# Kernel tuning notes

Hardware: AMD Instinct MI355X
Metric: run time of the kernel (lower is better)

## Reference

```python
import jax, jax.numpy as jnp
import numpy as np

DIM = 96
HEADS = 4
HID = int(DIM * 2.66)  # 255, GDFN hidden width
B, H, W = 4, 128, 128


def _conv(x, w, b=None, groups=1):
    y = jax.lax.conv_general_dilated(x, w, (1, 1), 'SAME',
                                     dimension_numbers=('NCHW', 'OIHW', 'NCHW'),
                                     feature_group_count=groups)
    return y if b is None else y + b[None, :, None, None]


def _ln(x, w, b):
    # WithBias LayerNorm over channel dim (per pixel), biased variance, eps=1e-5
    mu = x.mean(1, keepdims=True)
    var = ((x - mu) ** 2).mean(1, keepdims=True)
    return (x - mu) / jnp.sqrt(var + 1e-5) * w[None, :, None, None] + b[None, :, None, None]


def _l2norm(x):
    # torch F.normalize(dim=-1): x / max(||x||_2, 1e-12)
    return x / jnp.maximum(jnp.linalg.norm(x, axis=-1, keepdims=True), 1e-12)


def _gelu(x):
    return jax.nn.gelu(x, approximate=False)


def setup_inputs() -> dict:
    key = jax.random.key(0)
    ks = iter(jax.random.split(key, 32))
    nrm = lambda shp, s=0.02: jax.random.normal(next(ks), shp, dtype=jnp.float32) * s
    d, h2 = DIM, HID
    inp = {
        'x': jax.random.normal(next(ks), (B, DIM, H, W), dtype=jnp.float32),
        # L_conv: 3x3(d->d,+b) GELU 1x1(d->1,+b)
        'Lc_w1': nrm((d, d, 3, 3)), 'Lc_b1': jnp.zeros((d,), jnp.float32),
        'Lc_w2': nrm((1, d, 1, 1)), 'Lc_b2': jnp.zeros((1,), jnp.float32),
        # R_conv: 3x3(d->d,+b) GELU 1x1(d->3,+b)
        'Rc_w1': nrm((d, d, 3, 3)), 'Rc_b1': jnp.zeros((d,), jnp.float32),
        'Rc_w2': nrm((3, d, 1, 1)), 'Rc_b2': jnp.zeros((3,), jnp.float32),
        # L_rein: 3x3(1->d,+b) GELU ; R_rein: 3x3(3->d,+b)
        'Lr_w': nrm((d, 1, 3, 3)), 'Lr_b': jnp.zeros((d,), jnp.float32),
        'Rr_w': nrm((d, 3, 3, 3)), 'Rr_b': jnp.zeros((d,), jnp.float32),
        # LayerNorms (WithBias)
        'n1_w': jnp.ones((d,), jnp.float32), 'n1_b': jnp.zeros((d,), jnp.float32),
        'nL_w': jnp.ones((d,), jnp.float32), 'nL_b': jnp.zeros((d,), jnp.float32),
        'n2_w': jnp.ones((d,), jnp.float32), 'n2_b': jnp.zeros((d,), jnp.float32),
        # Illum_Attention (bias=False)
        'temp': jnp.ones((HEADS, 1, 1), jnp.float32),
        'q_w': nrm((d, d, 1, 1)),
        'qd_w': nrm((d, d, 3, 3)),          # q_dwconv is a FULL 3x3 conv (no groups)
        'kv_w': nrm((2 * d, d, 1, 1)),
        'kvd_w': nrm((2 * d, 1, 3, 3)),     # depthwise, groups=2*dim
        'po_w': nrm((d, d, 1, 1)),
        # FeedForward (bias=False); NOTE: 'dwconv' here is a FULL 3x3 conv
        'pi_w': nrm((h2, d, 1, 1)),
        'fdw_w': nrm((h2, h2, 3, 3)),
        'fpo_w': nrm((d, h2, 1, 1)),
    }
    return inp


def reference(x, Lc_w1, Lc_b1, Lc_w2, Lc_b2, Rc_w1, Rc_b1, Rc_w2, Rc_b2,
              Lr_w, Lr_b, Rr_w, Rr_b, n1_w, n1_b, nL_w, nL_b, n2_w, n2_b,
              temp, q_w, qd_w, kv_w, kvd_w, po_w, pi_w, fdw_w, fpo_w):
    b, c, h, w = x.shape
    # Retinex decomposition heads
    L = _conv(_gelu(_conv(x, Lc_w1, Lc_b1)), Lc_w2, Lc_b2)   # [b,1,h,w]
    R = _conv(_gelu(_conv(x, Rc_w1, Rc_b1)), Rc_w2, Rc_b2)   # [b,3,h,w]
    L_rein = _gelu(_conv(jax.lax.stop_gradient(L), Lr_w, Lr_b))  # detach in torch
    R_rein = _conv(jax.lax.stop_gradient(R), Rr_w, Rr_b)
    # Illum_Guided_TransformerBlock: x = x + attn(norm1(x), normL(illum))
    xn = _ln(x, n1_w, n1_b)
    ill = _ln(L_rein, nL_w, nL_b)
    q = _conv(_conv(ill, q_w), qd_w)
    kv = _conv(_conv(xn, kv_w), kvd_w, groups=2 * c)
    k, v = jnp.split(kv, 2, axis=1)
    ch, hw = c // HEADS, h * w
    heads = lambda t: t.reshape(b, HEADS, ch, hw)
    qh, kh, vh = _l2norm(heads(q)), _l2norm(heads(k)), heads(v)
    # channel-wise attention: [b,heads,ch,ch]
    attn = jax.nn.softmax(jnp.einsum('bhci,bhdi->bhcd', qh, kh) * temp[None], axis=-1)
    out = jnp.einsum('bhcd,bhdi->bhci', attn, vh).reshape(b, c, h, w)
    x = x + _conv(out, po_w)
    # x = x + ffn(norm2(x))
    x2 = _ln(x, n2_w, n2_b)
    x = x + _conv(_gelu(_conv(_conv(x2, pi_w), fdw_w)), fpo_w)
    x = x + R_rein
    return (x, L, R)
```

## Files before the change

kernel.cpp:

```cpp
#include <hip/hip_runtime.h>

#define HWsz 16384
#define Wd 128

typedef unsigned short ushortT;
typedef unsigned int uintT;
typedef __attribute__((ext_vector_type(8))) short short8v;
typedef __attribute__((ext_vector_type(4))) float f32x4;
typedef __attribute__((ext_vector_type(16))) float f32x16;
typedef __attribute__((ext_vector_type(4))) unsigned short ushort4v;

__device__ __forceinline__ float gelu_f(float x){
    return 0.5f * x * (1.0f + erff(x * 0.70710678118654752f));
}
__device__ __forceinline__ ushortT f2b(float f){
    union { float f; uintT u; } v; v.f = f;
    uintT r = v.u + 0x7FFFu + ((v.u >> 16) & 1u);
    return (ushortT)(r >> 16);
}
__device__ __forceinline__ float b2f(ushortT u){
    union { uintT u; float f; } v; v.u = ((uintT)u) << 16; return v.f;
}
__device__ __forceinline__ void gload_lds16(const ushortT* g, ushortT* l){
    __builtin_amdgcn_global_load_lds(
        (const __attribute__((address_space(1))) void*)g,
        (__attribute__((address_space(3))) void*)l, 16, 0, 0);
}

__device__ __forceinline__ void pack3_one(int e, const float* __restrict__ w,
    ushortT* __restrict__ outp, int cout, int cin, int BN, int NCH)
{
    int j = e & 7; int r = e >> 3;
    int ocl = r % BN; r /= BN;
    int kg  = r & 3;  r >>= 2;
    int tap = r % 9;  r /= 9;
    int ch  = r % NCH;
    int nt  = r / NCH;
    int ci = ch*32 + kg*8 + j;
    int oc = nt*BN + ocl;
    float v = (oc < cout && ci < cin) ? w[((size_t)oc*cin + ci)*9 + tap] : 0.f;
    outp[e] = f2b(v);
}
__device__ __forceinline__ void pack1_one(int e, const float* __restrict__ w,
    ushortT* __restrict__ outp, int cout, int cin, int BN, int NCH)
{
    int j = e & 7; int r = e >> 3;
    int ocl = r % BN; r /= BN;
    int kg  = r & 3;  r >>= 2;
    int ch  = r % NCH;
    int nt  = r / NCH;
    int ci = ch*32 + kg*8 + j;
    int oc = nt*BN + ocl;
    float v = (oc < cout && ci < cin) ? w[(size_t)oc*cin + ci] : 0.f;
    outp[e] = f2b(v);
}
__global__ __launch_bounds__(256) void pack_all_kernel(
    const float* Lc, const float* Rc, const float* Qd, const float* Fd,
    const float* Q1, const float* KV1, const float* PI1, const float* FPO1,
    ushortT* dL, ushortT* dR, ushortT* dQ, ushortT* dF,
    ushortT* dq0, ushortT* dkv, ushortT* dpi, ushortT* dfpo)
{
    int e = blockIdx.x*256 + threadIdx.x;
    if      (e < 82944)  pack3_one(e,        Lc, dL, 96, 96, 48, 3);
    else if (e < 165888) pack3_one(e-82944,  Rc, dR, 96, 96, 48, 3);
    else if (e < 248832) pack3_one(e-165888, Qd, dQ, 96, 96, 32, 3);
    else if (e < 838656) pack3_one(e-248832, Fd, dF, 255,255, 64, 8);
    else if (e < 847872) pack1_one(e-838656, Q1, dq0, 96, 96, 96, 3);
    else if (e < 866304) pack1_one(e-847872, KV1,dkv, 192,96, 48, 3);
    else if (e < 890880) pack1_one(e-866304, PI1,dpi, 255,96, 64, 3);
    else if (e < 915456) pack1_one(e-890880, FPO1,dfpo,96,255, 96, 8);
}

__global__ __launch_bounds__(256) void tonhwc_kernel(
    const float* __restrict__ in, ushortT* __restrict__ outp)
{
    const int p = blockIdx.x*256 + threadIdx.x;
    const int b = blockIdx.y;
    const float* ip = in + (size_t)b*96*HWsz + p;
    ushortT* op = outp + ((size_t)b*HWsz + p)*96;
#pragma unroll
    for (int g=0; g<12; g++){
        float v[8];
#pragma unroll
        for (int c=0;c<8;c++) v[c] = ip[(size_t)(g*8+c)*HWsz];
        uint4 pk;
        pk.x = (uintT)f2b(v[0]) | ((uintT)f2b(v[1])<<16);
        pk.y = (uintT)f2b(v[2]) | ((uintT)f2b(v[3])<<16);
        pk.z = (uintT)f2b(v[4]) | ((uintT)f2b(v[5])<<16);
        pk.w = (uintT)f2b(v[6]) | ((uintT)f2b(v[7])<<16);
        *(uint4*)(op + g*8) = pk;
    }
}

template<int NG, int NCH, int ACT, int TWOOUT>
__global__ __launch_bounds__(256,2) void conv3x3_v4(
    const ushortT* __restrict__ inh,
    const ushortT* __restrict__ wpk1, const ushortT* __restrict__ wpk2,
    const float* __restrict__ bias1, const float* __restrict__ bias2,
    ushortT* __restrict__ out1, ushortT* __restrict__ out2,
    int cout, int ocpad)
{
    constexpr int BN = NG*16;
    constexpr int Cpad = NCH*32;
    constexpr int WCH4 = 9*4*BN;
    constexpr int WI = (WCH4 + 255)/256;
    __shared__ __align__(16) ushortT As[4*324*8];
    __shared__ __align__(16) ushortT Ws[WCH4*8];

    const int tid = threadIdx.x;
    const int l   = tid & 63;
    const int wv  = tid >> 6;
    const int l15 = l & 15;
    const int kg  = l >> 4;
    const int tix = blockIdx.x & 7, tiy = blockIdx.x >> 3;
    const int b   = blockIdx.z;
    const int x0 = tix*16, y0 = tiy*16;

    int nt = blockIdx.y;
    const ushortT* wpk; const float* bias; ushortT* outp; int ntw;
    if (TWOOUT && nt >= 2){ wpk = wpk2; bias = bias2; outp = out2; ntw = nt-2; }
    else { wpk = wpk1; bias = bias1; outp = out1; ntw = nt; }
    const int ocbase = ntw*BN;

    f32x4 acc[4][NG];
#pragma unroll
    for (int m=0;m<4;m++)
#pragma unroll
        for (int n=0;n<NG;n++) acc[m][n] = (f32x4){0.f,0.f,0.f,0.f};

    const ushortT* inb = inh + (size_t)b*HWsz*Cpad;

    for (int ch=0; ch<NCH; ch++){
        __syncthreads();
        for (int t=tid; t<1296; t+=256){
            int p = t>>2, g = t&3;
            int hy = p/18, hx = p - hy*18;
            int gy = y0 + hy - 1, gx = x0 + hx - 1;
            uint4 v; v.x=0u; v.y=0u; v.z=0u; v.w=0u;
            if ((unsigned)gy < 128u && (unsigned)gx < 128u)
                v = *(const uint4*)(inb + (size_t)(gy*Wd+gx)*Cpad + ch*32 + g*8);
            *(uint4*)(As + (g*324+p)*8) = v;
        }
        {
            const ushortT* wsrc = wpk + ((size_t)ntw*NCH + ch)*(WCH4*8);
#pragma unroll
            for (int i=0; i<WI; i++){
                int t = i*256 + tid;
                if ((WCH4 & 255) == 0 || t < WCH4)
                    gload_lds16(wsrc + (size_t)t*8, Ws + (size_t)t*8);
            }
        }
        __syncthreads();
#pragma unroll
        for (int tp=0; tp<9; tp++){
            const int dy = tp/3, dx = tp - dy*3;
            short8v bf[NG];
#pragma unroll
            for (int n=0;n<NG;n++)
                bf[n] = *(const short8v*)(Ws + ((size_t)(tp*4 + kg)*BN + n*16 + l15)*8);
#pragma unroll
            for (int mg=0;mg<4;mg++){
                short8v a = *(const short8v*)(As + (kg*324 + (wv*4+mg+dy)*18 + l15+dx)*8);
#pragma unroll
                for (int n=0;n<NG;n++)
                    acc[mg][n] = __builtin_amdgcn_mfma_f32_16x16x32_bf16(a, bf[n], acc[mg][n], 0,0,0);
            }
        }
    }
    __syncthreads();
    ushortT* Ts = As + wv*1024;
#pragma unroll
    for (int mg=0;mg<4;mg++){
        int gy = y0 + wv*4 + mg;
        ushortT* orow = outp + ((size_t)b*HWsz + gy*Wd + x0)*ocpad + ocbase;
#pragma unroll
        for (int n=0;n<NG;n++){
            int ocl = n*16 + l15;
            int oc  = ocbase + ocl;
            float bs = (bias && oc < cout) ? bias[oc] : 0.f;
#pragma unroll
            for (int j=0;j<4;j++){
                int pxj = kg*4 + j;
                float r = 0.f;
                if (oc < cout){ r = acc[mg][n][j] + bs; if (ACT) r = gelu_f(r); }
                int seg = ((ocl>>3) + pxj) & 7;
                Ts[pxj*64 + seg*8 + (ocl&7)] = f2b(r);
            }
        }
#pragma unroll
        for (int ps=0; ps < (BN+31)/32; ps++){
            int rpx = l & 15;
            int rs  = (l>>4) + ps*4;
            if (rs*8 < BN){
                int pseg = (rs + rpx) & 7;
                short8v v = *(const short8v*)(Ts + rpx*64 + pseg*8);
                *(short8v*)(orow + (size_t)rpx*ocpad + rs*8) = v;
            }
        }
    }
}

template<int NGW, int NCH>
__global__ __launch_bounds__(256) void gemm1x1_v2(
    const ushortT* __restrict__ inh, const ushortT* __restrict__ wpk,
    ushortT* __restrict__ outp, int cout, int ocpad)
{
    constexpr int BN = NGW*16;
    constexpr int Cpad = NCH*32;
    __shared__ __align__(16) ushortT Ts[4*16*64];

    const int tid = threadIdx.x;
    const int l = tid & 63, wv = tid >> 6, l15 = l & 15, kg = l >> 4;
    const int p0 = blockIdx.x*64;
    const int b  = blockIdx.z;
    const int nt = wv, ocbase = wv*BN;
    const ushortT* inb = inh + (size_t)b*HWsz*Cpad;

    f32x4 acc[4][NGW];
#pragma unroll
    for (int m=0;m<4;m++)
#pragma unroll
        for (int n=0;n<NGW;n++) acc[m][n] = (f32x4){0.f,0.f,0.f,0.f};

#pragma unroll
    for (int ch=0; ch<NCH; ch++){
        short8v a[4], bw[NGW];
#pragma unroll
        for (int mg=0; mg<4; mg++)
            a[mg] = *(const short8v*)(inb + (size_t)(p0 + mg*16 + l15)*Cpad + ch*32 + kg*8);
#pragma unroll
        for (int n=0;n<NGW;n++)
            bw[n] = *(const short8v*)(wpk + (((size_t)(nt*NCH + ch)*4 + kg)*BN + n*16 + l15)*8);
#pragma unroll
        for (int mg=0;mg<4;mg++)
#pragma unroll
            for (int n=0;n<NGW;n++)
                acc[mg][n] = __builtin_amdgcn_mfma_f32_16x16x32_bf16(a[mg], bw[n], acc[mg][n], 0,0,0);
    }
    ushortT* Tw = Ts + wv*1024;
#pragma unroll
    for (int mg=0;mg<4;mg++){
        ushortT* orow = outp + ((size_t)b*HWsz + p0 + mg*16)*ocpad + ocbase;
#pragma unroll
        for (int n=0;n<NGW;n++){
            int ocl = n*16 + l15;
            int oc  = ocbase + ocl;
#pragma unroll
            for (int j=0;j<4;j++){
                int pxj = kg*4 + j;
                float r = (oc < cout) ? acc[mg][n][j] : 0.f;
                int seg = ((ocl>>3) + pxj) & 7;
                Tw[pxj*64 + seg*8 + (ocl&7)] = f2b(r);
            }
        }
#pragma unroll
        for (int ps=0; ps < (BN+31)/32; ps++){
            int rpx = l & 15;
            int rs  = (l>>4) + ps*4;
            if (rs*8 < BN){
                int pseg = (rs + rpx) & 7;
                short8v v = *(const short8v*)(Tw + rpx*64 + pseg*8);
                *(short8v*)(orow + (size_t)rpx*ocpad + rs*8) = v;
            }
        }
    }
}

template<int NG, int NCH, int ACT, int OMODE, int NSPLIT, int XMAP>
__global__ __launch_bounds__(256,4) void conv3x3_mfma(
    const ushortT* __restrict__ inh,
    const ushortT* __restrict__ wpk1, const ushortT* __restrict__ wpk2,
    const float* __restrict__ bias1, const float* __restrict__ bias2,
    void* __restrict__ out1, void* __restrict__ out2,
    int cout, int ocpad)
{
    constexpr int BN = NG*16;
    constexpr int Cpad = NCH*32;
    __shared__ __align__(16) ushortT As[4*324*8];

    const int tid = threadIdx.x;
    const int l   = tid & 63;
    const int wv  = tid >> 6;
    const int l15 = l & 15;
    const int kg  = l >> 4;
    int tile = blockIdx.x, nt = blockIdx.y, b = blockIdx.z;
    const int tix = tile & 7, tiy = tile >> 3;

    const ushortT* wpk = wpk1; const float* bias = bias1; void* outv = out1;
    if (NSPLIT > 0 && nt >= NSPLIT){ nt -= NSPLIT; wpk = wpk2; bias = bias2; outv = out2; }

    f32x4 acc[4][NG];
#pragma unroll
    for (int m=0;m<4;m++)
#pragma unroll
        for (int n=0;n<NG;n++) acc[m][n] = (f32x4){0.f,0.f,0.f,0.f};

    const ushortT* inb = inh + (size_t)b*HWsz*Cpad;

    for (int ch=0; ch<NCH; ch++){
        __syncthreads();
#pragma unroll
        for (int g=0; g<4; g++){
            for (int p=tid; p<324; p+=256){
                int hy = p/18, hx = p - hy*18;
                int gy = tiy*16 + hy - 1, gx = tix*16 + hx - 1;
                uint4 v; v.x=0u; v.y=0u; v.z=0u; v.w=0u;
                if ((unsigned)gy < 128u && (unsigned)gx < 128u)
                    v = *(const uint4*)(inb + (size_t)(gy*Wd+gx)*Cpad + ch*32 + g*8);
                *(uint4*)(As + (g*324+p)*8) = v;
            }
        }
        __syncthreads();
        const ushortT* wch = wpk + (size_t)(nt*NCH + ch)*(9*4*BN*8);
#pragma unroll
        for (int tp=0; tp<9; tp++){
            const int dy = tp/3, dx = tp - dy*3;
            short8v a[4], bf[NG];
#pragma unroll
            for (int mg=0; mg<4; mg++){
                int p = (wv*4 + mg + dy)*18 + l15 + dx;
                a[mg] = *(const short8v*)(As + (kg*324 + p)*8);
            }
#pragma unroll
            for (int n=0;n<NG;n++)
                bf[n] = *(const short8v*)(wch + ((size_t)(tp*4 + kg)*BN + n*16 + l15)*8);
#pragma unroll
            for (int mg=0;mg<4;mg++)
#pragma unroll
                for (int n=0;n<NG;n++)
                    acc[mg][n] = __builtin_amdgcn_mfma_f32_16x16x32_bf16(a[mg], bf[n], acc[mg][n], 0,0,0);
        }
    }
    if (OMODE == 2){
        ushortT* out = (ushortT*)outv;
#pragma unroll
        for (int n=0;n<NG;n++){
            int oc = nt*BN + n*16 + l15;
            if (oc < cout){
                float bs = bias ? bias[oc] : 0.f;
#pragma unroll
                for (int mg=0;mg<4;mg++){
                    int gy = tiy*16 + wv*4 + mg;
                    int gx = tix*16 + kg*4;
                    ushort4v pk;
#pragma unroll
                    for (int j=0;j<4;j++){
                        float r = acc[mg][n][j] + bs;
                        if (ACT) r = gelu_f(r);
                        pk[j] = f2b(r);
                    }
                    *(ushort4v*)(out + ((size_t)b*cout + oc)*HWsz + gy*Wd + gx) = pk;
                }
            }
        }
    }
}

template<int NG, int NCH, int RES, int OMODE, int XMAP>
__global__ __launch_bounds__(256) void gemm1x1_mfma(
    const ushortT* __restrict__ inh, const ushortT* __restrict__ wpk, int wstride_z,
    const float* __restrict__ res1, const ushortT* __restrict__ res2b,
    void* __restrict__ outv, int cout, int ocpad)
{
    constexpr int BN = NG*16;
    constexpr int Cpad = NCH*32;
    constexpr int LSTR = (BN <= 64) ? 64 : 128;
    constexpr int MASK = LSTR/8 - 1;
    __shared__ __align__(16) ushortT TsS[(OMODE==1) ? 4*16*LSTR : 16];

    const int tid = threadIdx.x;
    const int l = tid & 63, wv = tid >> 6, l15 = l & 15, kg = l >> 4;
    int chunk = blockIdx.x, nt = blockIdx.y, b = blockIdx.z;
    const int p0 = chunk*256 + wv*64;
    const ushortT* inb = inh + (size_t)b*HWsz*Cpad;
    const ushortT* wp  = wpk + (size_t)b*wstride_z;

    f32x4 acc[4][NG];
#pragma unroll
    for (int m=0;m<4;m++)
#pragma unroll
        for (int n=0;n<NG;n++) acc[m][n] = (f32x4){0.f,0.f,0.f,0.f};

#pragma unroll
    for (int ch=0; ch<NCH; ch++){
        short8v a[4], bw[NG];
#pragma unroll
        for (int mg=0; mg<4; mg++)
            a[mg] = *(const short8v*)(inb + (size_t)(p0 + mg*16 + l15)*Cpad + ch*32 + kg*8);
#pragma unroll
        for (int n=0;n<NG;n++)
            bw[n] = *(const short8v*)(wp + (((size_t)(nt*NCH + ch)*4 + kg)*BN + n*16 + l15)*8);
#pragma unroll
        for (int mg=0;mg<4;mg++)
#pragma unroll
            for (int n=0;n<NG;n++)
                acc[mg][n] = __builtin_amdgcn_mfma_f32_16x16x32_bf16(a[mg], bw[n], acc[mg][n], 0,0,0);
    }
    if (OMODE == 0){
        float* out = (float*)outv;
#pragma unroll
        for (int n=0;n<NG;n++){
            int oc = nt*BN + n*16 + l15;
            if (oc < cout){
#pragma unroll
                for (int mg=0;mg<4;mg++){
                    int pix = p0 + mg*16 + kg*4;
                    size_t idx = ((size_t)b*cout + oc)*HWsz + pix;
                    float4 r;
                    r.x = acc[mg][n][0]; r.y = acc[mg][n][1];
                    r.z = acc[mg][n][2]; r.w = acc[mg][n][3];
                    if (RES>=1){ float4 q = *(const float4*)(res1+idx); r.x+=q.x;r.y+=q.y;r.z+=q.z;r.w+=q.w; }
                    if (RES>=2){
                        ushort4v q = *(const ushort4v*)(res2b+idx);
                        r.x+=b2f(q[0]); r.y+=b2f(q[1]); r.z+=b2f(q[2]); r.w+=b2f(q[3]);
                    }
                    *(float4*)(out + idx) = r;
                }
            }
        }
    } else {
        ushortT* outp = (ushortT*)outv;
        ushortT* Ts = TsS + wv*(16*LSTR);
#pragma unroll
        for (int mg=0;mg<4;mg++){
            ushortT* orow = outp + ((size_t)b*HWsz + p0 + mg*16)*ocpad + nt*BN;
#pragma unroll
            for (int n=0;n<NG;n++){
                int ocl = n*16 + l15;
                int oc  = nt*BN + ocl;
#pragma unroll
                for (int j=0;j<4;j++){
                    int pxj = kg*4 + j;
                    float r = (oc < cout) ? acc[mg][n][j] : 0.f;
                    int seg = ((ocl>>3) + pxj) & MASK;
                    Ts[pxj*LSTR + seg*8 + (ocl&7)] = f2b(r);
                }
            }
#pragma unroll
            for (int ps=0; ps < (BN+31)/32; ps++){
                int rpx = l & 15;
                int rs  = (l>>4) + ps*4;
                if (rs*8 < BN){
                    int pseg = (rs + rpx) & MASK;
                    short8v v = *(const short8v*)(Ts + rpx*LSTR + pseg*8);
                    *(short8v*)(orow + (size_t)rpx*ocpad + rs*8) = v;
                }
            }
        }
    }
}

template<int NOUT>
__global__ __launch_bounds__(256) void head1x1_kernel(
    const ushortT* __restrict__ inh, const float* __restrict__ w,
    const float* __restrict__ bias, float* __restrict__ out)
{
    __shared__ float lw[NOUT*96];
    const int tid = threadIdx.x;
    for (int t=tid; t<NOUT*96; t+=256) lw[t] = w[t];
    __syncthreads();
    const int p = blockIdx.x*256 + tid;
    const int b = blockIdx.y;
    const ushortT* ip = inh + ((size_t)b*HWsz + p)*96;
    float v[96];
#pragma unroll
    for (int g=0; g<12; g++){
        short8v s = *(const short8v*)(ip + g*8);
#pragma unroll
        for (int i=0;i<8;i++) v[g*8+i] = b2f((ushortT)s[i]);
    }
#pragma unroll
    for (int oc=0; oc<NOUT; oc++){
        float acc = bias[oc];
#pragma unroll
        for (int c=0;c<96;c++) acc += v[c]*lw[oc*96+c];
        out[((size_t)b*NOUT + oc)*HWsz + p] = acc;
    }
}

__global__ __launch_bounds__(256) void lrein_ln_kernel(
    const float* __restrict__ L, const float* __restrict__ w,
    const float* __restrict__ bias, const float* __restrict__ lnw,
    const float* __restrict__ lnb, ushortT* __restrict__ outh)
{
    __shared__ float sw[864], sb[96], sn1[96], sn2[96];
    const int tid = threadIdx.x;
    for (int t=tid; t<864; t+=256) sw[t] = w[t];
    if (tid < 96){ sb[tid]=bias[tid]; sn1[tid]=lnw[tid]; sn2[tid]=lnb[tid]; }
    __syncthreads();
    const int p = blockIdx.x*256 + tid;
    const int b = blockIdx.y;
    const int y = p>>7, x = p&127;
    const float* ib = L + (size_t)b*HWsz;
    float win[9];
#pragma unroll
    for (int dy=0;dy<3;dy++)
#pragma unroll
        for (int dx=0;dx<3;dx++){
            int gy=y+dy-1, gx=x+dx-1;
            win[dy*3+dx] = ((unsigned)gy<128u && (unsigned)gx<128u) ? ib[gy*Wd+gx] : 0.f;
        }
    float v[96]; float s=0.f;
#pragma unroll
    for (int c=0;c<96;c++){
        float a = sb[c];
#pragma unroll
        for (int t=0;t<9;t++) a += win[t]*sw[c*9+t];
        a = gelu_f(a);
        v[c]=a; s+=a;
    }
    const float mu = s*(1.f/96.f);
    float s2=0.f;
#pragma unroll
    for (int c=0;c<96;c++){ float d=v[c]-mu; s2+=d*d; }
    const float inv = 1.f/sqrtf(s2*(1.f/96.f)+1e-5f);
    ushortT* op = outh + ((size_t)b*HWsz + p)*96;
#pragma unroll
    for (int g=0; g<12; g++){
        uint4 pk; uintT w4[4];
#pragma unroll
        for (int i=0;i<4;i++){
            float r0 = (v[g*8+2*i]-mu)*inv*sn1[g*8+2*i]+sn2[g*8+2*i];
            float r1 = (v[g*8+2*i+1]-mu)*inv*sn1[g*8+2*i+1]+sn2[g*8+2*i+1];
            w4[i] = (uintT)f2b(r0) | ((uintT)f2b(r1)<<16);
        }
        pk.x=w4[0]; pk.y=w4[1]; pk.z=w4[2]; pk.w=w4[3];
        *(uint4*)(op + g*8) = pk;
    }
}

__global__ __launch_bounds__(256) void ln_n2n_kernel(
    const float* __restrict__ in, const float* __restrict__ w,
    const float* __restrict__ bias, ushortT* __restrict__ outh)
{
    const int p = blockIdx.x*256+threadIdx.x;
    const int b = blockIdx.y;
    const float* ip = in + (size_t)b*96*HWsz + p;
    float v[96]; float s=0.f;
#pragma unroll
    for(int c=0;c<96;c++){ v[c]=ip[(size_t)c*HWsz]; s+=v[c]; }
    const float mu = s*(1.f/96.f);
    float s2=0.f;
#pragma unroll
    for(int c=0;c<96;c++){ float d=v[c]-mu; s2+=d*d; }
    const float inv = 1.f/sqrtf(s2*(1.f/96.f)+1e-5f);
    ushortT* op = outh + ((size_t)b*HWsz + p)*96;
#pragma unroll
    for (int g=0; g<12; g++){
        uint4 pk; uintT w4[4];
#pragma unroll
        for (int i=0;i<4;i++){
            float r0 = (v[g*8+2*i]-mu)*inv*w[g*8+2*i]+bias[g*8+2*i];
            float r1 = (v[g*8+2*i+1]-mu)*inv*w[g*8+2*i+1]+bias[g*8+2*i+1];
            w4[i] = (uintT)f2b(r0) | ((uintT)f2b(r1)<<16);
        }
        pk.x=w4[0]; pk.y=w4[1]; pk.z=w4[2]; pk.w=w4[3];
        *(uint4*)(op + g*8) = pk;
    }
}

__global__ __launch_bounds__(256) void conv3x3_rr_kernel(
    const float* __restrict__ in, const float* __restrict__ w,
    const float* __restrict__ bias, ushortT* __restrict__ out)
{
    __shared__ float sw[216], sb[8];
    const int oc0 = blockIdx.y*8;
    if (threadIdx.x < 216) sw[threadIdx.x] = w[(size_t)oc0*27 + threadIdx.x];
    if (threadIdx.x < 8)   sb[threadIdx.x] = bias[oc0 + threadIdx.x];
    __syncthreads();
    const int p = blockIdx.x*256+threadIdx.x;
    const int b = blockIdx.z;
    const int y=p>>7, x=p&127;
    const float* ib = in + (size_t)b*3*HWsz;
    float win[27];
#pragma unroll
    for (int ci=0;ci<3;ci++)
#pragma unroll
        for (int dy=0;dy<3;dy++)
#pragma unroll
            for (int dx=0;dx<3;dx++){
                int gy=y+dy-1, gx=x+dx-1;
                win[ci*9+dy*3+dx] = ((unsigned)gy<128u && (unsigned)gx<128u)
                    ? ib[(size_t)ci*HWsz + gy*Wd+gx] : 0.f;
            }
#pragma unroll
    for (int i=0;i<8;i++){
        float acc = sb[i];
#pragma unroll
        for (int t=0;t<27;t++) acc += win[t]*sw[i*27+t];
        out[((size_t)b*96 + oc0+i)*HWsz + p] = f2b(acc);
    }
}

__global__ __launch_bounds__(256) void dw_nhwc_kernel(
    const ushortT* __restrict__ inh, const float* __restrict__ w,
    ushortT* __restrict__ kout, ushortT* __restrict__ vouth)
{
    const int p = blockIdx.x*256+threadIdx.x;
    const int c0 = blockIdx.y*8;
    const int b = blockIdx.z;
    const int y=p>>7, x=p&127;
    float lw[72];
#pragma unroll
    for (int i=0;i<8;i++)
#pragma unroll
        for (int t=0;t<9;t++) lw[i*9+t] = w[(size_t)(c0+i)*9 + t];
    const ushortT* ib = inh + (size_t)b*HWsz*192;
    float acc[8];
#pragma unroll
    for (int i=0;i<8;i++) acc[i]=0.f;
#pragma unroll
    for(int dy=0;dy<3;dy++){
        int gy=y+dy-1;
        if((unsigned)gy<128u){
#pragma unroll
            for(int dx=0;dx<3;dx++){
                int gx=x+dx-1;
                if((unsigned)gx<128u){
                    short8v s = *(const short8v*)(ib + (size_t)(gy*Wd+gx)*192 + c0);
#pragma unroll
                    for (int i=0;i<8;i++) acc[i] += b2f((ushortT)s[i])*lw[i*9+dy*3+dx];
                }
            }
        }
    }
    if (c0 < 96){
#pragma unroll
        for (int i=0;i<8;i++)
            kout[((size_t)b*96 + c0+i)*HWsz + p] = f2b(acc[i]);
    } else {
        ushortT* op = vouth + ((size_t)b*HWsz + p)*96 + (c0-96);
        uint4 pk;
        pk.x = (uintT)f2b(acc[0]) | ((uintT)f2b(acc[1])<<16);
        pk.y = (uintT)f2b(acc[2]) | ((uintT)f2b(acc[3])<<16);
        pk.z = (uintT)f2b(acc[4]) | ((uintT)f2b(acc[5])<<16);
        pk.w = (uintT)f2b(acc[6]) | ((uintT)f2b(acc[7])<<16);
        *(uint4*)op = pk;
    }
}

__global__ __launch_bounds__(256) void rownorm_bf16_kernel(
    const ushortT* __restrict__ qb, const ushortT* __restrict__ kb,
    float* __restrict__ invqk)
{
    __shared__ float red[256];
    const int r = blockIdx.x;
    const ushortT* ip = (r < 384) ? (qb + (size_t)r*HWsz) : (kb + (size_t)(r-384)*HWsz);
    float s=0.f;
    const ushortT* tp = ip + threadIdx.x*64;
#pragma unroll
    for (int g=0; g<8; g++){
        short8v v = *(const short8v*)(tp + g*8);
#pragma unroll
        for (int i=0;i<8;i++){ float f = b2f((ushortT)v[i]); s += f*f; }
    }
    red[threadIdx.x]=s; __syncthreads();
    for(int st=128; st>0; st>>=1){
        if(threadIdx.x<st) red[threadIdx.x]+=red[threadIdx.x+st];
        __syncthreads();
    }
    if(threadIdx.x==0) invqk[r] = 1.f/fmaxf(sqrtf(red[0]), 1e-12f);
}

__global__ __launch_bounds__(256) void qk_mfma_kernel(
    const ushortT* __restrict__ qb, const ushortT* __restrict__ kb,
    float* __restrict__ part)
{
    const int tid = threadIdx.x;
    const int l = tid & 63, wv = tid >> 6;
    const int chunk = blockIdx.x*4 + wv;
    const int bh = blockIdx.y, b = bh>>2, h = bh&3;
    const int ch = min(l & 31, 23);
    const int kh = (l >> 5)*8;
    const ushortT* qp = qb + ((size_t)b*96 + h*24 + ch)*HWsz + chunk*512 + kh;
    const ushortT* kp = kb + ((size_t)b*96 + h*24 + ch)*HWsz + chunk*512 + kh;
    f32x16 acc;
#pragma unroll
    for (int r=0;r<16;r++) acc[r]=0.f;
    for (int ks=0; ks<32; ks++){
        short8v a  = *(const short8v*)(qp + ks*16);
        short8v bb = *(const short8v*)(kp + ks*16);
        acc = __builtin_amdgcn_mfma_f32_32x32x16_bf16(a, bb, acc, 0,0,0);
    }
    float* op = part + ((size_t)chunk*16 + bh)*1024;
    const int col = l & 31;
#pragma unroll
    for (int r=0;r<16;r++){
        int row = (r&3) + 8*(r>>2) + 4*(l>>5);
        op[row*32 + col] = acc[r];
    }
}

__global__ void qk_reduce_kernel(const float* __restrict__ part, float* __restrict__ out)
{
    int idx = blockIdx.x*256+threadIdx.x;
    float s=0.f;
    for(int c=0;c<32;c++) s += part[(size_t)c*16384 + idx];
    out[idx]=s;
}

__global__ __launch_bounds__(576) void softmax_kernel(
    const float* __restrict__ raw, const float* __restrict__ invq,
    const float* __restrict__ invk, const float* __restrict__ temp,
    float* __restrict__ attn)
{
    __shared__ float l[576];
    const int bh=blockIdx.x, b=bh>>2, h=bh&3;
    const int tid=threadIdx.x;
    const int i=tid/24, j=tid-i*24;
    l[tid] = raw[(size_t)bh*1024 + i*32 + j] * invq[b*96+h*24+i] * invk[b*96+h*24+j] * temp[h];
    __syncthreads();
    if(tid<24){
        float m=-1e30f;
#pragma unroll
        for(int jj=0;jj<24;jj++) m = fmaxf(m, l[tid*24+jj]);
        float e[24]; float s=0.f;
#pragma unroll
        for(int jj=0;jj<24;jj++){ e[jj]=__expf(l[tid*24+jj]-m); s+=e[jj]; }
        float isv = 1.f/s;
#pragma unroll
        for(int jj=0;jj<24;jj++) attn[(size_t)bh*576 + tid*24 + jj] = e[jj]*isv;
    }
}

__global__ __launch_bounds__(256) void mkM_kernel(
    const float* __restrict__ attn, const float* __restrict__ po_w,
    ushortT* __restrict__ Mpk)
{
    const int b = blockIdx.x;
    for (int e = threadIdx.x; e < 9216; e += 256){
        int oc = e / 96, d = e - oc*96;
        int h = d / 24, dl = d - h*24;
        const float* aw = attn + ((size_t)(b*4+h))*576 + dl;
        const float* pw = po_w + (size_t)oc*96 + h*24;
        float s = 0.f;
#pragma unroll
        for (int c=0;c<24;c++) s += pw[c]*aw[c*24];
        int ch = d>>5, kg = (d>>3)&3, j = d&7;
        Mpk[(size_t)b*9216 + ((size_t)(ch*4+kg)*96 + oc)*8 + j] = f2b(s);
    }
}

extern "C" void kernel_launch(void* const* d_in, const int* in_sizes, int n_in,
                              void* d_out, int out_size, void* d_ws, size_t ws_size,
                              hipStream_t stream)
{
    const float* x     = (const float*)d_in[0];
    const float* Lc_w1 = (const float*)d_in[1];
    const float* Lc_b1 = (const float*)d_in[2];
    const float* Lc_w2 = (const float*)d_in[3];
    const float* Lc_b2 = (const float*)d_in[4];
    const float* Rc_w1 = (const float*)d_in[5];
    const float* Rc_b1 = (const float*)d_in[6];
    const float* Rc_w2 = (const float*)d_in[7];
    const float* Rc_b2 = (const float*)d_in[8];
    const float* Lr_w  = (const float*)d_in[9];
    const float* Lr_b  = (const float*)d_in[10];
    const float* Rr_w  = (const float*)d_in[11];
    const float* Rr_b  = (const float*)d_in[12];
    const float* n1_w  = (const float*)d_in[13];
    const float* n1_b  = (const float*)d_in[14];
    const float* nL_w  = (const float*)d_in[15];
    const float* nL_b  = (const float*)d_in[16];
    const float* n2_w  = (const float*)d_in[17];
    const float* n2_b  = (const float*)d_in[18];
    const float* temp  = (const float*)d_in[19];
    const float* q_w   = (const float*)d_in[20];
    const float* qd_w  = (const float*)d_in[21];
    const float* kv_w  = (const float*)d_in[22];
    const float* kvd_w = (const float*)d_in[23];
    const float* po_w  = (const float*)d_in[24];
    const float* pi_w  = (const float*)d_in[25];
    const float* fdw_w = (const float*)d_in[26];
    const float* fpo_w = (const float*)d_in[27];

    char* base = (char*)d_ws;
    ushortT* xh   = (ushortT*)(base + 0);
    ushortT* f0h  = (ushortT*)(base + 0);
    ushortT* Lh   = (ushortT*)(base + 33554432);
    ushortT* kv0h = (ushortT*)(base + 33554432);
    ushortT* f1h  = (ushortT*)(base + 33554432);
    ushortT* Rh   = (ushortT*)(base + 67108864);
    ushortT* vh   = (ushortT*)(base + 67108864);
    ushortT* x2nh = (ushortT*)(base + 67108864);
    ushortT* illh = (ushortT*)(base + 79691776);
    ushortT* xnh  = (ushortT*)(base + 92274688);
    ushortT* q0h  = (ushortT*)(base + 104857600);
    ushortT* qb   = (ushortT*)(base + 117440512);
    float*   x1   = (float*)(base + 117440512);
    ushortT* kb   = (ushortT*)(base + 142606336);
    ushortT* Bb   = (ushortT*)(base + 155189248);
    char* smb = base + 167772160;
    ushortT* wpkL = (ushortT*)smb;   smb += 165888;
    ushortT* wpkR = (ushortT*)smb;   smb += 165888;
    ushortT* wpkQ = (ushortT*)smb;   smb += 165888;
    ushortT* wpkF = (ushortT*)smb;   smb += 1179648;
    ushortT* wq0  = (ushortT*)smb;   smb += 18432;
    ushortT* wkv  = (ushortT*)smb;   smb += 36864;
    ushortT* wpi  = (ushortT*)smb;   smb += 49152;
    ushortT* wfpo = (ushortT*)smb;   smb += 49152;
    ushortT* Mpk  = (ushortT*)smb;   smb += 73728;
    float* invqk  = (float*)smb;     smb += 3072;
    float* part   = (float*)smb;     smb += 2097152;
    float* araw   = (float*)smb;     smb += 65536;
    float* attn   = (float*)smb;     smb += 36864;

    float* out_x = (float*)d_out;
    float* out_L = out_x + (size_t)4*96*HWsz;
    float* out_R = out_L + (size_t)4*HWsz;

    dim3 blk(256);

    hipLaunchKernelGGL(pack_all_kernel, dim3(3576), blk, 0, stream,
        Lc_w1, Rc_w1, qd_w, fdw_w, q_w, kv_w, pi_w, fpo_w,
        wpkL, wpkR, wpkQ, wpkF, wq0, wkv, wpi, wfpo);
    hipLaunchKernelGGL(tonhwc_kernel, dim3(64,4), blk, 0, stream, x, xh);

    hipLaunchKernelGGL((conv3x3_v4<3,3,1,1>), dim3(64,4,4), blk, 0, stream,
        xh, wpkL, wpkR, Lc_b1, Rc_b1, Lh, Rh, 96, 96);
    hipLaunchKernelGGL((head1x1_kernel<1>), dim3(64,4), blk, 0, stream, Lh, Lc_w2, Lc_b2, out_L);
    hipLaunchKernelGGL((head1x1_kernel<3>), dim3(64,4), blk, 0, stream, Rh, Rc_w2, Rc_b2, out_R);
    hipLaunchKernelGGL(lrein_ln_kernel, dim3(64,4), blk, 0, stream, out_L, Lr_w, Lr_b, nL_w, nL_b, illh);
    hipLaunchKernelGGL(conv3x3_rr_kernel, dim3(64,12,4), blk, 0, stream, out_R, Rr_w, Rr_b, Bb);

    hipLaunchKernelGGL(ln_n2n_kernel, dim3(64,4), blk, 0, stream, x, n1_w, n1_b, xnh);

    hipLaunchKernelGGL((gemm1x1_mfma<6,3,0,1,0>), dim3(64,1,4), blk, 0, stream,
        illh, wq0, 0, nullptr, nullptr, (void*)q0h, 96, 96);
    hipLaunchKernelGGL((conv3x3_mfma<2,3,0,2,0,0>), dim3(64,3,4), blk, 0, stream,
        q0h, wpkQ, wpkQ, nullptr, nullptr, (void*)qb, (void*)qb, 96, 0);
    hipLaunchKernelGGL((gemm1x1_v2<3,3>), dim3(256,1,4), blk, 0, stream,
        xnh, wkv, kv0h, 192, 192);
    hipLaunchKernelGGL(dw_nhwc_kernel, dim3(64,24,4), blk, 0, stream, kv0h, kvd_w, kb, vh);

    hipLaunchKernelGGL(rownorm_bf16_kernel, dim3(768), blk, 0, stream, qb, kb, invqk);
    hipLaunchKernelGGL(qk_mfma_kernel, dim3(8,16), blk, 0, stream, qb, kb, part);
    hipLaunchKernelGGL(qk_reduce_kernel, dim3(64), blk, 0, stream, part, araw);
    hipLaunchKernelGGL(softmax_kernel, dim3(16), dim3(576), 0, stream, araw, invqk, invqk+384, temp, attn);
    hipLaunchKernelGGL(mkM_kernel, dim3(4), blk, 0, stream, attn, po_w, Mpk);
    hipLaunchKernelGGL((gemm1x1_mfma<6,3,1,0,0>), dim3(64,1,4), blk, 0, stream,
        vh, Mpk, 9216, x, nullptr, (void*)x1, 96, 0);

    hipLaunchKernelGGL(ln_n2n_kernel, dim3(64,4), blk, 0, stream, x1, n2_w, n2_b, x2nh);
    hipLaunchKernelGGL((gemm1x1_v2<4,3>), dim3(256,1,4), blk, 0, stream,
        x2nh, wpi, f0h, 255, 256);
    hipLaunchKernelGGL((conv3x3_v4<4,8,1,0>), dim3(64,4,4), blk, 0, stream,
        f0h, wpkF, wpkF, nullptr, nullptr, f1h, f1h, 255, 256);
    hipLaunchKernelGGL((gemm1x1_mfma<6,8,2,0,0>), dim3(64,1,4), blk, 0, stream,
        f1h, wfpo, 0, x1, Bb, (void*)out_x, 96, 0);
}
```

Before: 376.9 us.

## Widen conv3x3 spatial tile to 32x16 pixels for better weight reuse

The 3x3 MFMA conv kernel now covers a 32-wide by 16-tall pixel tile per block instead of 16x16, so each lane computes two horizontal halves. Each weight fragment loaded from LDS feeds twice as many MFMAs, and the halo overhead per output pixel drops. In exchange the accumulator count doubles, which raises register pressure and may hurt occupancy at launch_bounds(256,2). The grid shrinks to 32 tiles per image, which lowers the total block count.

```diff
diff --git a/kernel.cpp b/kernel.cpp
--- a/kernel.cpp
+++ b/kernel.cpp
@@ -93,7 +93,7 @@
 }
 
 template<int NG, int NCH, int ACT, int TWOOUT>
-__global__ __launch_bounds__(256,2) void conv3x3_v4(
+__global__ __launch_bounds__(256,2) void conv3x3_v5(
     const ushortT* __restrict__ inh,
     const ushortT* __restrict__ wpk1, const ushortT* __restrict__ wpk2,
     const float* __restrict__ bias1, const float* __restrict__ bias2,
@@ -102,9 +102,10 @@
 {
     constexpr int BN = NG*16;
     constexpr int Cpad = NCH*32;
+    constexpr int HALO = 612;
     constexpr int WCH4 = 9*4*BN;
     constexpr int WI = (WCH4 + 255)/256;
-    __shared__ __align__(16) ushortT As[4*324*8];
+    __shared__ __align__(16) ushortT As[4*HALO*8];
     __shared__ __align__(16) ushortT Ws[WCH4*8];
 
     const int tid = threadIdx.x;
@@ -112,9 +113,9 @@
     const int wv  = tid >> 6;
     const int l15 = l & 15;
     const int kg  = l >> 4;
-    const int tix = blockIdx.x & 7, tiy = blockIdx.x >> 3;
+    const int tix = blockIdx.x & 3, tiy = blockIdx.x >> 2;
     const int b   = blockIdx.z;
-    const int x0 = tix*16, y0 = tiy*16;
+    const int x0 = tix*32, y0 = tiy*16;
 
     int nt = blockIdx.y;
     const ushortT* wpk; const float* bias; ushortT* outp; int ntw;
@@ -122,24 +123,28 @@
     else { wpk = wpk1; bias = bias1; outp = out1; ntw = nt; }
     const int ocbase = ntw*BN;
 
-    f32x4 acc[4][NG];
+    f32x4 acc[4][2][NG];
 #pragma unroll
     for (int m=0;m<4;m++)
 #pragma unroll
-        for (int n=0;n<NG;n++) acc[m][n] = (f32x4){0.f,0.f,0.f,0.f};
+        for (int hf=0;hf<2;hf++)
+#pragma unroll
+            for (int n=0;n<NG;n++) acc[m][hf][n] = (f32x4){0.f,0.f,0.f,0.f};
 
     const ushortT* inb = inh + (size_t)b*HWsz*Cpad;
 
     for (int ch=0; ch<NCH; ch++){
         __syncthreads();
-        for (int t=tid; t<1296; t+=256){
-            int p = t>>2, g = t&3;
-            int hy = p/18, hx = p - hy*18;
-            int gy = y0 + hy - 1, gx = x0 + hx - 1;
-            uint4 v; v.x=0u; v.y=0u; v.z=0u; v.w=0u;
-            if ((unsigned)gy < 128u && (unsigned)gx < 128u)
-                v = *(const uint4*)(inb + (size_t)(gy*Wd+gx)*Cpad + ch*32 + g*8);
-            *(uint4*)(As + (g*324+p)*8) = v;
+#pragma unroll
+        for (int g=0; g<4; g++){
+            for (int p=tid; p<HALO; p+=256){
+                int hy = p/34, hx = p - hy*34;
+                int gy = y0 + hy - 1, gx = x0 + hx - 1;
+                uint4 v; v.x=0u; v.y=0u; v.z=0u; v.w=0u;
+                if ((unsigned)gy < 128u && (unsigned)gx < 128u)
+                    v = *(const uint4*)(inb + (size_t)(gy*Wd+gx)*Cpad + ch*32 + g*8);
+                *(uint4*)(As + (g*HALO+p)*8) = v;
+            }
         }
         {
             const ushortT* wsrc = wpk + ((size_t)ntw*NCH + ch)*(WCH4*8);
@@ -160,38 +165,45 @@
                 bf[n] = *(const short8v*)(Ws + ((size_t)(tp*4 + kg)*BN + n*16 + l15)*8);
 #pragma unroll
             for (int mg=0;mg<4;mg++){
-                short8v a = *(const short8v*)(As + (kg*324 + (wv*4+mg+dy)*18 + l15+dx)*8);
-#pragma unroll
-                for (int n=0;n<NG;n++)
-                    acc[mg][n] = __builtin_amdgcn_mfma_f32_16x16x32_bf16(a, bf[n], acc[mg][n], 0,0,0);
+#pragma unroll
+                for (int hf=0;hf<2;hf++){
+                    short8v a = *(const short8v*)(As + (kg*HALO + (wv*4+mg+dy)*34 + hf*16 + l15+dx)*8);
+#pragma unroll
+                    for (int n=0;n<NG;n++)
+                        acc[mg][hf][n] = __builtin_amdgcn_mfma_f32_16x16x32_bf16(a, bf[n], acc[mg][hf][n], 0,0,0);
+                }
             }
         }
     }
     __syncthreads();
-    ushortT* Ts = As + wv*1024;
+    ushortT* Ts = As + wv*2048;
+    constexpr int NSEG = BN/8;
 #pragma unroll
     for (int mg=0;mg<4;mg++){
         int gy = y0 + wv*4 + mg;
         ushortT* orow = outp + ((size_t)b*HWsz + gy*Wd + x0)*ocpad + ocbase;
 #pragma unroll
-        for (int n=0;n<NG;n++){
-            int ocl = n*16 + l15;
-            int oc  = ocbase + ocl;
-            float bs = (bias && oc < cout) ? bias[oc] : 0.f;
-#pragma unroll
-            for (int j=0;j<4;j++){
-                int pxj = kg*4 + j;
-                float r = 0.f;
-                if (oc < cout){ r = acc[mg][n][j] + bs; if (ACT) r = gelu_f(r); }
-                int seg = ((ocl>>3) + pxj) & 7;
-                Ts[pxj*64 + seg*8 + (ocl&7)] = f2b(r);
-            }
-        }
-#pragma unroll
-        for (int ps=0; ps < (BN+31)/32; ps++){
-            int rpx = l & 15;
-            int rs  = (l>>4) + ps*4;
-            if (rs*8 < BN){
+        for (int hf=0;hf<2;hf++){
+#pragma unroll
+            for (int n=0;n<NG;n++){
+                int ocl = n*16 + l15;
+                int oc  = ocbase + ocl;
+                float bs = (bias && oc < cout) ? bias[oc] : 0.f;
+#pragma unroll
+                for (int j=0;j<4;j++){
+                    int px = hf*16 + kg*4 + j;
+                    float r = 0.f;
+                    if (oc < cout){ r = acc[mg][hf][n][j] + bs; if (ACT) r = gelu_f(r); }
+                    int seg = ((ocl>>3) + px) & 7;
+                    Ts[px*64 + seg*8 + (ocl&7)] = f2b(r);
+                }
+            }
+        }
+#pragma unroll
+        for (int ps=0; ps < (NSEG+1)/2; ps++){
+            int rpx = l & 31;
+            int rs  = (l>>5) + ps*2;
+            if (rs < NSEG){
                 int pseg = (rs + rpx) & 7;
                 short8v v = *(const short8v*)(Ts + rpx*64 + pseg*8);
                 *(short8v*)(orow + (size_t)rpx*ocpad + rs*8) = v;
@@ -816,7 +828,7 @@
         wpkL, wpkR, wpkQ, wpkF, wq0, wkv, wpi, wfpo);
     hipLaunchKernelGGL(tonhwc_kernel, dim3(64,4), blk, 0, stream, x, xh);
 
-    hipLaunchKernelGGL((conv3x3_v4<3,3,1,1>), dim3(64,4,4), blk, 0, stream,
+    hipLaunchKernelGGL((conv3x3_v5<3,3,1,1>), dim3(32,4,4), blk, 0, stream,
         xh, wpkL, wpkR, Lc_b1, Rc_b1, Lh, Rh, 96, 96);
     hipLaunchKernelGGL((head1x1_kernel<1>), dim3(64,4), blk, 0, stream, Lh, Lc_w2, Lc_b2, out_L);
     hipLaunchKernelGGL((head1x1_kernel<3>), dim3(64,4), blk, 0, stream, Rh, Rc_w2, Rc_b2, out_R);
@@ -844,7 +856,7 @@
     hipLaunchKernelGGL(ln_n2n_kernel, dim3(64,4), blk, 0, stream, x1, n2_w, n2_b, x2nh);
     hipLaunchKernelGGL((gemm1x1_v2<4,3>), dim3(256,1,4), blk, 0, stream,
         x2nh, wpi, f0h, 255, 256);
-    hipLaunchKernelGGL((conv3x3_v4<4,8,1,0>), dim3(64,4,4), blk, 0, stream,
+    hipLaunchKernelGGL((conv3x3_v5<4,8,1,0>), dim3(32,4,4), blk, 0, stream,
         f0h, wpkF, wpkF, nullptr, nullptr, f1h, f1h, 255, 256);
     hipLaunchKernelGGL((gemm1x1_mfma<6,8,2,0,0>), dim3(64,1,4), blk, 0, stream,
         f1h, wfpo, 0, x1, Bb, (void*)out_x, 96, 0);
```

New measurement: 390.1 us. +3.5%, slower.
